# Kernel tuning notes

Measured on AMD Instinct MI355X. Metric: run time of the kernel, lower is better.

Reference implementation:

```python
import jax, jax.numpy as jnp
import numpy as np

R, TR = 47, 2  # response_size, treat_size


def _lstm_cell(x, h, c, Wih, Whh, bih, bhh):
    # PyTorch gate order: i, f, g, o
    gates = x @ Wih.T + h @ Whh.T + bih + bhh
    i, f, g, o = jnp.split(gates, 4, axis=-1)
    c_new = jax.nn.sigmoid(f) * c + jax.nn.sigmoid(i) * jnp.tanh(g)
    h_new = jax.nn.sigmoid(o) * jnp.tanh(c_new)
    return h_new, c_new


def setup_inputs() -> dict:
    key = jax.random.key(0)
    B, T = 256, 2048
    ks = jax.random.split(key, 20)

    def u(k, shape, H):
        s = 1.0 / np.sqrt(H).astype(np.float32)
        return jax.random.uniform(k, shape, jnp.float32, -s, s)

    return {
        "x_r": jax.random.normal(ks[0], (B, T, R), jnp.float32),
        "x_t": jax.random.normal(ks[1], (B, T, TR), jnp.float32),
        # r_rnn: 2-layer LSTM, input 49 -> hidden 47
        "r_Wih0": u(ks[2], (4 * R, R + TR), R), "r_Whh0": u(ks[3], (4 * R, R), R),
        "r_bih0": u(ks[4], (4 * R,), R), "r_bhh0": u(ks[5], (4 * R,), R),
        "r_Wih1": u(ks[6], (4 * R, R), R), "r_Whh1": u(ks[7], (4 * R, R), R),
        "r_bih1": u(ks[8], (4 * R,), R), "r_bhh1": u(ks[9], (4 * R,), R),
        # t_rnn: 2-layer LSTM, input 96 -> hidden 2
        "t_Wih0": u(ks[10], (4 * TR, 2 * R + TR), TR), "t_Whh0": u(ks[11], (4 * TR, TR), TR),
        "t_bih0": u(ks[12], (4 * TR,), TR), "t_bhh0": u(ks[13], (4 * TR,), TR),
        "t_Wih1": u(ks[14], (4 * TR, TR), TR), "t_Whh1": u(ks[15], (4 * TR, TR), TR),
        "t_bih1": u(ks[16], (4 * TR,), TR), "t_bhh1": u(ks[17], (4 * TR,), TR),
    }


def reference(x_r, x_t,
              r_Wih0, r_Whh0, r_bih0, r_bhh0, r_Wih1, r_Whh1, r_bih1, r_bhh1,
              t_Wih0, t_Whh0, t_bih0, t_bhh0, t_Wih1, t_Whh1, t_bih1, t_bhh1):
    B = x_r.shape[0]
    zR = jnp.zeros((B, R), x_r.dtype)
    zT = jnp.zeros((B, TR), x_r.dtype)

    def step(carry, xs):
        hr0, cr0, hr1, cr1, ht0, ct0, ht1, ct1 = carry
        r, t = xs  # [B,47], [B,2]
        r_in = jnp.concatenate([r, t], axis=-1)              # [B,49]
        hr0, cr0 = _lstm_cell(r_in, hr0, cr0, r_Wih0, r_Whh0, r_bih0, r_bhh0)
        hr1, cr1 = _lstm_cell(hr0, hr1, cr1, r_Wih1, r_Whh1, r_bih1, r_bhh1)
        t_in = jnp.concatenate([r_in, hr1], axis=-1)         # [B,96]
        ht0, ct0 = _lstm_cell(t_in, ht0, ct0, t_Wih0, t_Whh0, t_bih0, t_bhh0)
        ht1, ct1 = _lstm_cell(ht0, ht1, ct1, t_Wih1, t_Whh1, t_bih1, t_bhh1)
        return (hr0, cr0, hr1, cr1, ht0, ct0, ht1, ct1), (hr1, ht1)

    init = (zR, zR, zR, zR, zT, zT, zT, zT)
    xs = (x_r.transpose(1, 0, 2), x_t.transpose(1, 0, 2))    # time-major
    _, (r_seq, t_seq) = jax.lax.scan(step, init, xs)         # [T,B,47], [T,B,2]
    return (r_seq.transpose(1, 0, 2), t_seq.transpose(1, 0, 2))
```

## Files before the change

### kernel.cpp

```cpp
#include <hip/hip_runtime.h>

#define T_STEPS 2048
#define TOTAL   2080

typedef float f2 __attribute__((ext_vector_type(2)));
typedef _Float16 h2 __attribute__((ext_vector_type(2)));

__device__ __forceinline__ float fast_rcp(float x) { return __builtin_amdgcn_rcpf(x); }

__device__ __forceinline__ float sig_f(float x) { return fast_rcp(1.0f + __expf(-x)); }
__device__ __forceinline__ float tanh_f(float x) {
    float e = __expf(-2.0f * x);
    return fmaf(2.0f, fast_rcp(1.0f + e), -1.0f);
}
__device__ __forceinline__ float gate_act(float x, float zm, float sm, float sa) {
    float e = __expf(-x * zm);
    return fmaf(fast_rcp(1.0f + e), sm, sa);
}

#if __has_builtin(__builtin_amdgcn_fdot2)
#define FDOT2(a, b, c) __builtin_amdgcn_fdot2((a), (b), (c), false)
#else
__device__ __forceinline__ float FDOT2(h2 a, h2 b, float c) {
    return fmaf((float)a.x, (float)b.x, fmaf((float)a.y, (float)b.y, c));
}
#endif

#define LDS_BARRIER() asm volatile("s_waitcnt lgkmcnt(0)\n\ts_barrier" ::: "memory")

#define DPP_BCAST0 0x00
#define DPP_BCAST1 0x55
#define DPP_BCAST2 0xAA
#define DPP_BCAST3 0xFF
#define DPP_PAIR   0xF5
#define DPP_ROR4   0x124
#define DPP_ROR8   0x128
template<int CTRL>
__device__ __forceinline__ float dppf(float x) {
    int r = __builtin_amdgcn_update_dpp(0, __builtin_bit_cast(int, x), CTRL, 0xF, 0xF, true);
    return __builtin_bit_cast(float, r);
}

__device__ __forceinline__ void loadx4(float (&dst)[4], const float* __restrict__ x_r,
                                       const float* __restrict__ x_t,
                                       size_t xrb, size_t xtb, int l) {
#pragma unroll
    for (int u = 0; u < 4; ++u) {
        int v = l + 16 * u;
        dst[u] = (v < 47) ? x_r[xrb + v] : ((v < 49) ? x_t[xtb + (v - 47)] : 0.0f);
    }
}

__device__ __forceinline__ void unpack12(f2 (&in)[24], const float4* __restrict__ r4) {
#pragma unroll
    for (int u = 0; u < 12; ++u) {
        float4 v = r4[u];
        in[2 * u]     = f2{v.x, v.y};
        in[2 * u + 1] = f2{v.z, v.w};
    }
}

__device__ __forceinline__ void unpackh(h2 (&in)[24], const h2* __restrict__ row) {
    const float4* q = (const float4*)row;
#pragma unroll
    for (int k = 0; k < 6; ++k) {
        float4 v = q[k];
        in[4 * k + 0] = __builtin_bit_cast(h2, v.x);
        in[4 * k + 1] = __builtin_bit_cast(h2, v.y);
        in[4 * k + 2] = __builtin_bit_cast(h2, v.z);
        in[4 * k + 3] = __builtin_bit_cast(h2, v.w);
    }
}

__device__ __forceinline__ float4 dot4h(const h2 (&in)[24], const h2 (&w)[4][24], float4 init) {
    float a0 = init.x, a1 = init.y, a2 = init.z, a3 = init.w;
#pragma unroll
    for (int u = 0; u < 24; ++u) {
        a0 = FDOT2(w[0][u], in[u], a0);
        a1 = FDOT2(w[1][u], in[u], a1);
        a2 = FDOT2(w[2][u], in[u], a2);
        a3 = FDOT2(w[3][u], in[u], a3);
    }
    return float4{a0, a1, a2, a3};
}

__device__ __forceinline__ void loadw47h(h2 (&w)[24], const float* __restrict__ src) {
#pragma unroll
    for (int u = 0; u < 23; ++u)
        w[u] = h2{(_Float16)src[2 * u], (_Float16)src[2 * u + 1]};
    w[23] = h2{(_Float16)src[46], (_Float16)0.0f};
}

__global__ __launch_bounds__(256) void adrnn_fused(
    const float* __restrict__ x_r, const float* __restrict__ x_t,
    const float* __restrict__ rWih0, const float* __restrict__ rWhh0,
    const float* __restrict__ rbih0, const float* __restrict__ rbhh0,
    const float* __restrict__ rWih1, const float* __restrict__ rWhh1,
    const float* __restrict__ rbih1, const float* __restrict__ rbhh1,
    const float* __restrict__ tWih0, const float* __restrict__ tWhh0,
    const float* __restrict__ tbih0, const float* __restrict__ tbhh0,
    const float* __restrict__ tWih1, const float* __restrict__ tWhh1,
    const float* __restrict__ tbih1, const float* __restrict__ tbhh1,
    float* __restrict__ r_out, float* __restrict__ t_out)
{
    __shared__ __align__(16) float tring[64][112];
    __shared__ __align__(16) h2 h0f16[16][32];
    __shared__ __align__(16) h2 h1f16[16][32];
    __shared__ __align__(16) float pAring[16][192];
    __shared__ __align__(16) float pBring[16][192];

    const int tid = threadIdx.x;
    const int wid = tid >> 6;
    const int l   = tid & 63;
    const int j   = l;
    const int b = blockIdx.x;
    const size_t xr_base = (size_t)b * T_STEPS * 47;
    const size_t xt_base = (size_t)b * T_STEPS * 2;

    {
        for (int k = tid; k < 64 * 48; k += 256) tring[k / 48][64 + (k % 48)] = 0.0f;
        for (int k = tid; k < 16 * 32; k += 256) {
            h0f16[k >> 5][k & 31] = h2{(_Float16)0.0f, (_Float16)0.0f};
            h1f16[k >> 5][k & 31] = h2{(_Float16)0.0f, (_Float16)0.0f};
        }
    }

    if (wid == 0) {
        f2 w[4][24]; float w48[4]; float4 bias = {0, 0, 0, 0};
#pragma unroll
        for (int g = 0; g < 4; ++g) { w48[g] = 0.f;
#pragma unroll
            for (int u = 0; u < 24; ++u) w[g][u] = f2{0.f, 0.f}; }
        if (j < 47) {
            float bb[4];
#pragma unroll
            for (int g = 0; g < 4; ++g) {
                const int row = g * 47 + j;
#pragma unroll
                for (int u = 0; u < 24; ++u)
                    w[g][u] = f2{rWih0[row * 49 + 2 * u], rWih0[row * 49 + 2 * u + 1]};
                w48[g] = rWih0[row * 49 + 48];
                bb[g] = rbih0[row] + rbhh0[row];
            }
            bias = {bb[0], bb[1], bb[2], bb[3]};
        }
        float xa[4] = {0,0,0,0}, xb[4] = {0,0,0,0}, xc[4] = {0,0,0,0};
        if (l < 16) {
            for (int t = 0; t < 8; ++t) {
                float xv[4];
                loadx4(xv, x_r, x_t, xr_base + (size_t)t * 47, xt_base + (size_t)t * 2, l);
#pragma unroll
                for (int uu = 0; uu < 4; ++uu) {
                    int v = l + 16 * uu;
                    if (v < 49) tring[t][v] = xv[uu];
                }
            }
            loadx4(xa, x_r, x_t, xr_base + (size_t)8 * 47,  xt_base + (size_t)8 * 2,  l);
            loadx4(xb, x_r, x_t, xr_base + (size_t)9 * 47,  xt_base + (size_t)9 * 2,  l);
            loadx4(xc, x_r, x_t, xr_base + (size_t)10 * 47, xt_base + (size_t)10 * 2, l);
        }
        __syncthreads();
        for (int i = 0; i < TOTAL; ++i) {
            if (i < T_STEPS && j < 47) {
                f2 in[24];
                unpack12(in, (const float4*)&tring[i & 63][0]);
                float x48 = tring[i & 63][48];
                f2 a0 = f2{bias.x, 0.f}, b0v = {0, 0};
                f2 a1 = f2{bias.y, 0.f}, b1v = {0, 0};
                f2 a2 = f2{bias.z, 0.f}, b2v = {0, 0};
                f2 a3 = f2{bias.w, 0.f}, b3v = {0, 0};
#pragma unroll
                for (int u = 0; u < 12; ++u) {
                    a0  = __builtin_elementwise_fma(w[0][u],      in[u],      a0);
                    b0v = __builtin_elementwise_fma(w[0][12 + u], in[12 + u], b0v);
                    a1  = __builtin_elementwise_fma(w[1][u],      in[u],      a1);
                    b1v = __builtin_elementwise_fma(w[1][12 + u], in[12 + u], b1v);
                    a2  = __builtin_elementwise_fma(w[2][u],      in[u],      a2);
                    b2v = __builtin_elementwise_fma(w[2][12 + u], in[12 + u], b2v);
                    a3  = __builtin_elementwise_fma(w[3][u],      in[u],      a3);
                    b3v = __builtin_elementwise_fma(w[3][12 + u], in[12 + u], b3v);
                }
                f2 s0 = a0 + b0v, s1 = a1 + b1v, s2 = a2 + b2v, s3 = a3 + b3v;
                float4 out;
                out.x = fmaf(w48[0], x48, s0.x + s0.y);
                out.y = fmaf(w48[1], x48, s1.x + s1.y);
                out.z = fmaf(w48[2], x48, s2.x + s2.y);
                out.w = fmaf(w48[3], x48, s3.x + s3.y);
                *(float4*)&pAring[i & 15][j * 4] = out;
            }
            if (l < 16) {
                const int tw = i + 8;
                if (tw < T_STEPS) {
#pragma unroll
                    for (int uu = 0; uu < 4; ++uu) {
                        int v = l + 16 * uu;
                        if (v < 49) tring[tw & 63][v] = xa[uu];
                    }
                }
#pragma unroll
                for (int uu = 0; uu < 4; ++uu) { xa[uu] = xb[uu]; xb[uu] = xc[uu]; }
                int tl = i + 11;
                if (tl > T_STEPS - 1) tl = T_STEPS - 1;
                loadx4(xc, x_r, x_t, xr_base + (size_t)tl * 47, xt_base + (size_t)tl * 2, l);
            }
            if ((i & 7) == 7) LDS_BARRIER();
        }
    } else if (wid == 1) {
        h2 w[4][24];
#pragma unroll
        for (int g = 0; g < 4; ++g)
#pragma unroll
            for (int u = 0; u < 24; ++u) w[g][u] = h2{(_Float16)0.0f, (_Float16)0.0f};
        if (j < 47) {
#pragma unroll
            for (int g = 0; g < 4; ++g) loadw47h(w[g], &rWhh0[(g * 47 + j) * 47]);
        }
        float c0 = 0.f;
        __syncthreads();
        for (int i = 0; i < TOTAL; ++i) {
            const int s = i - 8;
            float hv = 0.0f;
            if (s >= 0 && s < T_STEPS && j < 47) {
                float4 pa = *(const float4*)&pAring[s & 15][j * 4];
                h2 in[24];
                unpackh(in, &h0f16[(s - 1) & 15][0]);
                float4 pre = dot4h(in, w, pa);
                float iv = sig_f(pre.x), fv = sig_f(pre.y);
                float gv = tanh_f(pre.z), ov = sig_f(pre.w);
                c0 = fmaf(fv, c0, iv * gv);
                hv = ov * tanh_f(c0);
            }
            float hn = dppf<DPP_PAIR>(hv);
            if (s >= 0 && s < T_STEPS && j < 47 && !(j & 1)) {
                h0f16[s & 15][j >> 1] = __builtin_bit_cast(h2, __builtin_amdgcn_cvt_pkrtz(hv, hn));
            }
            if ((i & 7) == 7) LDS_BARRIER();
        }
    } else if (wid == 2) {
        h2 w[4][24]; float4 bias = {0, 0, 0, 0};
#pragma unroll
        for (int g = 0; g < 4; ++g)
#pragma unroll
            for (int u = 0; u < 24; ++u) w[g][u] = h2{(_Float16)0.0f, (_Float16)0.0f};
        if (j < 47) {
            float bb[4];
#pragma unroll
            for (int g = 0; g < 4; ++g) {
                loadw47h(w[g], &rWih1[(g * 47 + j) * 47]);
                bb[g] = rbih1[g * 47 + j] + rbhh1[g * 47 + j];
            }
            bias = {bb[0], bb[1], bb[2], bb[3]};
        }
        const int tu  = (l >> 2) & 1;
        const int tg  = l & 3;
        const int thf = (l >> 3) & 1;
        const int R0 = tg * 2 + tu;
        f2 wt[24]; float wx48;
        if (thf == 0) {
            wx48 = 0.f;
#pragma unroll
            for (int k = 0; k < 24; ++k)
                wt[k] = f2{tWih0[R0 * 96 + 2 * k], tWih0[R0 * 96 + 2 * k + 1]};
        } else {
            wx48 = tWih0[R0 * 96 + 48];
#pragma unroll
            for (int k = 0; k < 23; ++k)
                wt[k] = f2{tWih0[R0 * 96 + 49 + 2 * k], tWih0[R0 * 96 + 49 + 2 * k + 1]};
            wt[23] = f2{tWih0[R0 * 96 + 95], 0.f};
        }
        const float bT0 = tbih0[R0] + tbhh0[R0];
        const float wh00 = tWhh0[R0 * 2 + 0], wh01 = tWhh0[R0 * 2 + 1];
        const float wi10 = tWih1[R0 * 2 + 0], wi11 = tWih1[R0 * 2 + 1];
        const float wh10 = tWhh1[R0 * 2 + 0], wh11 = tWhh1[R0 * 2 + 1];
        const float bT1 = tbih1[R0] + tbhh1[R0];
        const bool isg = (tg == 2);
        const float zm = isg ? 2.f : 1.f, sm = isg ? 2.f : 1.f, sa = isg ? -1.f : 0.f;
        float ht00 = 0.f, ht01 = 0.f, ct0u = 0.f;
        float ht10 = 0.f, ht11 = 0.f, ct1u = 0.f;

        __syncthreads();
        for (int i = 0; i < TOTAL; ++i) {
            const int s2 = i - 16;
            if (s2 >= 0 && s2 < T_STEPS && j < 47) {
                h2 in[24];
                unpackh(in, &h0f16[s2 & 15][0]);
                float4 pre = dot4h(in, w, bias);
                *(float4*)&pBring[s2 & 15][j * 4] = pre;
            }
            const int s = i - 32;
            if (s >= 0 && s < T_STEPS) {
                f2 in[24];
                unpack12(in, (const float4*)&tring[s & 63][thf ? 64 : 0]);
                float x48 = tring[s & 63][48];
                f2 av = {0, 0}, bv = {0, 0};
#pragma unroll
                for (int k = 0; k < 12; ++k) {
                    av = __builtin_elementwise_fma(wt[2 * k],     in[2 * k],     av);
                    bv = __builtin_elementwise_fma(wt[2 * k + 1], in[2 * k + 1], bv);
                }
                f2 sv = av + bv;
                float part = fmaf(wx48, x48, sv.x + sv.y);
                float pre0 = part + dppf<DPP_ROR8>(part);
                pre0 += bT0 + wh00 * ht00 + wh01 * ht01;
                float a0 = gate_act(pre0, zm, sm, sa);
                float i0 = dppf<DPP_BCAST0>(a0);
                float f0 = dppf<DPP_BCAST1>(a0);
                float g0 = dppf<DPP_BCAST2>(a0);
                float o0 = dppf<DPP_BCAST3>(a0);
                ct0u = fmaf(f0, ct0u, i0 * g0);
                float htu = o0 * tanh_f(ct0u);
                float hto = dppf<DPP_ROR4>(htu);
                ht00 = (tu == 0) ? htu : hto;
                ht01 = (tu == 0) ? hto : htu;
                float pre1 = bT1 + wi10 * ht00 + wi11 * ht01 + wh10 * ht10 + wh11 * ht11;
                float a1 = gate_act(pre1, zm, sm, sa);
                float ji = dppf<DPP_BCAST0>(a1);
                float jf = dppf<DPP_BCAST1>(a1);
                float jg = dppf<DPP_BCAST2>(a1);
                float jo = dppf<DPP_BCAST3>(a1);
                ct1u = fmaf(jf, ct1u, ji * jg);
                float h1u = jo * tanh_f(ct1u);
                float h1o = dppf<DPP_ROR4>(h1u);
                ht10 = (tu == 0) ? h1u : h1o;
                ht11 = (tu == 0) ? h1o : h1u;
                if (l == 0) {
                    float2 tv = {ht10, ht11};
                    *reinterpret_cast<float2*>(&t_out[((size_t)b * T_STEPS + s) * 2]) = tv;
                }
            }
            if ((i & 7) == 7) LDS_BARRIER();
        }
    } else {
        h2 w[4][24];
#pragma unroll
        for (int g = 0; g < 4; ++g)
#pragma unroll
            for (int u = 0; u < 24; ++u) w[g][u] = h2{(_Float16)0.0f, (_Float16)0.0f};
        if (j < 47) {
#pragma unroll
            for (int g = 0; g < 4; ++g) loadw47h(w[g], &rWhh1[(g * 47 + j) * 47]);
        }
        float c1 = 0.f;
        __syncthreads();
        for (int i = 0; i < TOTAL; ++i) {
            const int s = i - 24;
            float hv = 0.0f;
            if (s >= 0 && s < T_STEPS && j < 47) {
                float4 pb = *(const float4*)&pBring[s & 15][j * 4];
                h2 in[24];
                unpackh(in, &h1f16[(s - 1) & 15][0]);
                float4 pre = dot4h(in, w, pb);
                float iv = sig_f(pre.x), fv = sig_f(pre.y);
                float gv = tanh_f(pre.z), ov = sig_f(pre.w);
                c1 = fmaf(fv, c1, iv * gv);
                hv = ov * tanh_f(c1);
                tring[s & 63][64 + j] = hv;
                r_out[((size_t)b * T_STEPS + s) * 47 + j] = hv;
            }
            float hn = dppf<DPP_PAIR>(hv);
            if (s >= 0 && s < T_STEPS && j < 47 && !(j & 1)) {
                h1f16[s & 15][j >> 1] = __builtin_bit_cast(h2, __builtin_amdgcn_cvt_pkrtz(hv, hn));
            }
            if ((i & 7) == 7) LDS_BARRIER();
        }
    }
}

extern "C" void kernel_launch(void* const* d_in, const int* in_sizes, int n_in,
                              void* d_out, int out_size, void* d_ws, size_t ws_size,
                              hipStream_t stream) {
    const float* x_r   = (const float*)d_in[0];
    const float* x_t   = (const float*)d_in[1];
    const float* rWih0 = (const float*)d_in[2];
    const float* rWhh0 = (const float*)d_in[3];
    const float* rbih0 = (const float*)d_in[4];
    const float* rbhh0 = (const float*)d_in[5];
    const float* rWih1 = (const float*)d_in[6];
    const float* rWhh1 = (const float*)d_in[7];
    const float* rbih1 = (const float*)d_in[8];
    const float* rbhh1 = (const float*)d_in[9];
    const float* tWih0 = (const float*)d_in[10];
    const float* tWhh0 = (const float*)d_in[11];
    const float* tbih0 = (const float*)d_in[12];
    const float* tbhh0 = (const float*)d_in[13];
    const float* tWih1 = (const float*)d_in[14];
    const float* tWhh1 = (const float*)d_in[15];
    const float* tbih1 = (const float*)d_in[16];
    const float* tbhh1 = (const float*)d_in[17];

    float* r_out = (float*)d_out;
    float* t_out = r_out + (size_t)256 * T_STEPS * 47;

    hipLaunchKernelGGL(adrnn_fused, dim3(256), dim3(256), 0, stream,
                       x_r, x_t, rWih0, rWhh0, rbih0, rbhh0, rWih1, rWhh1, rbih1, rbhh1,
                       tWih0, tWhh0, tbih0, tbhh0, tWih1, tWhh1, tbih1, tbhh1,
                       r_out, t_out);
}
```

Measured before the change: 1.452 ms.

## Collapse four-wave LSTM pipeline into three waves with fused per-layer dot products

Restructures the block from four wavefronts (input projection, layer-0 recurrence, layer-1 input projection, layer-1 recurrence plus t_rnn) into three. Each r_rnn layer wave now computes both its input and hidden products itself in fp16 fdot2, and the t_rnn wave also handles the x prefetch ring, now stored as packed fp16. This removes the pAring/pBring staging buffers and shortens the pipeline depth (TOTAL 2080 to 2064). The cost is a longer serial dependency chain per layer step and extra fp16 rounding of inputs and of the t_rnn weights.

```diff
diff --git a/kernel.cpp b/kernel.cpp
--- a/kernel.cpp
+++ b/kernel.cpp
@@ -1,13 +1,12 @@
 #include <hip/hip_runtime.h>
 
 #define T_STEPS 2048
-#define TOTAL   2080
+#define TOTAL   2064
 
 typedef float f2 __attribute__((ext_vector_type(2)));
 typedef _Float16 h2 __attribute__((ext_vector_type(2)));
 
 __device__ __forceinline__ float fast_rcp(float x) { return __builtin_amdgcn_rcpf(x); }
-
 __device__ __forceinline__ float sig_f(float x) { return fast_rcp(1.0f + __expf(-x)); }
 __device__ __forceinline__ float tanh_f(float x) {
     float e = __expf(-2.0f * x);
@@ -41,23 +40,8 @@
     return __builtin_bit_cast(float, r);
 }
 
-__device__ __forceinline__ void loadx4(float (&dst)[4], const float* __restrict__ x_r,
-                                       const float* __restrict__ x_t,
-                                       size_t xrb, size_t xtb, int l) {
-#pragma unroll
-    for (int u = 0; u < 4; ++u) {
-        int v = l + 16 * u;
-        dst[u] = (v < 47) ? x_r[xrb + v] : ((v < 49) ? x_t[xtb + (v - 47)] : 0.0f);
-    }
-}
-
-__device__ __forceinline__ void unpack12(f2 (&in)[24], const float4* __restrict__ r4) {
-#pragma unroll
-    for (int u = 0; u < 12; ++u) {
-        float4 v = r4[u];
-        in[2 * u]     = f2{v.x, v.y};
-        in[2 * u + 1] = f2{v.z, v.w};
-    }
+__device__ __forceinline__ h2 pk16(float a, float b) {
+    return __builtin_bit_cast(h2, __builtin_amdgcn_cvt_pkrtz(a, b));
 }
 
 __device__ __forceinline__ void unpackh(h2 (&in)[24], const h2* __restrict__ row) {
@@ -71,17 +55,16 @@
         in[4 * k + 3] = __builtin_bit_cast(h2, v.w);
     }
 }
-
-__device__ __forceinline__ float4 dot4h(const h2 (&in)[24], const h2 (&w)[4][24], float4 init) {
-    float a0 = init.x, a1 = init.y, a2 = init.z, a3 = init.w;
-#pragma unroll
-    for (int u = 0; u < 24; ++u) {
-        a0 = FDOT2(w[0][u], in[u], a0);
-        a1 = FDOT2(w[1][u], in[u], a1);
-        a2 = FDOT2(w[2][u], in[u], a2);
-        a3 = FDOT2(w[3][u], in[u], a3);
-    }
-    return float4{a0, a1, a2, a3};
+__device__ __forceinline__ void unpackx(h2 (&in)[28], const h2* __restrict__ row) {
+    const float4* q = (const float4*)row;
+#pragma unroll
+    for (int k = 0; k < 7; ++k) {
+        float4 v = q[k];
+        in[4 * k + 0] = __builtin_bit_cast(h2, v.x);
+        in[4 * k + 1] = __builtin_bit_cast(h2, v.y);
+        in[4 * k + 2] = __builtin_bit_cast(h2, v.z);
+        in[4 * k + 3] = __builtin_bit_cast(h2, v.w);
+    }
 }
 
 __device__ __forceinline__ void loadw47h(h2 (&w)[24], const float* __restrict__ src) {
@@ -90,8 +73,24 @@
         w[u] = h2{(_Float16)src[2 * u], (_Float16)src[2 * u + 1]};
     w[23] = h2{(_Float16)src[46], (_Float16)0.0f};
 }
-
-__global__ __launch_bounds__(256) void adrnn_fused(
+__device__ __forceinline__ void loadw49h(h2 (&w)[25], const float* __restrict__ src) {
+#pragma unroll
+    for (int u = 0; u < 24; ++u)
+        w[u] = h2{(_Float16)src[2 * u], (_Float16)src[2 * u + 1]};
+    w[24] = h2{(_Float16)src[48], (_Float16)0.0f};
+}
+
+__device__ __forceinline__ void loadx4c(float (&dst)[4], const float* __restrict__ x_r,
+                                        const float* __restrict__ x_t,
+                                        size_t xrb, size_t xtb, int k) {
+#pragma unroll
+    for (int m = 0; m < 4; ++m) {
+        int v = 4 * k + m;
+        dst[m] = (v < 47) ? x_r[xrb + v] : ((v < 49) ? x_t[xtb + (v - 47)] : 0.0f);
+    }
+}
+
+__global__ __launch_bounds__(192) void adrnn_fused(
     const float* __restrict__ x_r, const float* __restrict__ x_t,
     const float* __restrict__ rWih0, const float* __restrict__ rWhh0,
     const float* __restrict__ rbih0, const float* __restrict__ rbhh0,
@@ -103,11 +102,9 @@
     const float* __restrict__ tbih1, const float* __restrict__ tbhh1,
     float* __restrict__ r_out, float* __restrict__ t_out)
 {
-    __shared__ __align__(16) float tring[64][112];
-    __shared__ __align__(16) h2 h0f16[16][32];
-    __shared__ __align__(16) h2 h1f16[16][32];
-    __shared__ __align__(16) float pAring[16][192];
-    __shared__ __align__(16) float pBring[16][192];
+    __shared__ __align__(16) h2 xring[32][28];
+    __shared__ __align__(16) h2 h0f16[16][24];
+    __shared__ __align__(16) h2 h1f16[16][24];
 
     const int tid = threadIdx.x;
     const int wid = tid >> 6;
@@ -117,156 +114,133 @@
     const size_t xr_base = (size_t)b * T_STEPS * 47;
     const size_t xt_base = (size_t)b * T_STEPS * 2;
 
-    {
-        for (int k = tid; k < 64 * 48; k += 256) tring[k / 48][64 + (k % 48)] = 0.0f;
-        for (int k = tid; k < 16 * 32; k += 256) {
-            h0f16[k >> 5][k & 31] = h2{(_Float16)0.0f, (_Float16)0.0f};
-            h1f16[k >> 5][k & 31] = h2{(_Float16)0.0f, (_Float16)0.0f};
-        }
+    for (int k = tid; k < 16 * 24; k += 192) {
+        h0f16[k / 24][k % 24] = h2{(_Float16)0.0f, (_Float16)0.0f};
+        h1f16[k / 24][k % 24] = h2{(_Float16)0.0f, (_Float16)0.0f};
     }
 
     if (wid == 0) {
-        f2 w[4][24]; float w48[4]; float4 bias = {0, 0, 0, 0};
-#pragma unroll
-        for (int g = 0; g < 4; ++g) { w48[g] = 0.f;
-#pragma unroll
-            for (int u = 0; u < 24; ++u) w[g][u] = f2{0.f, 0.f}; }
+        h2 wx[4][25]; h2 wh[4][24]; float bias[4] = {0, 0, 0, 0};
+#pragma unroll
+        for (int g = 0; g < 4; ++g) {
+#pragma unroll
+            for (int u = 0; u < 25; ++u) wx[g][u] = h2{(_Float16)0.0f, (_Float16)0.0f};
+#pragma unroll
+            for (int u = 0; u < 24; ++u) wh[g][u] = h2{(_Float16)0.0f, (_Float16)0.0f};
+        }
         if (j < 47) {
-            float bb[4];
 #pragma unroll
             for (int g = 0; g < 4; ++g) {
                 const int row = g * 47 + j;
-#pragma unroll
-                for (int u = 0; u < 24; ++u)
-                    w[g][u] = f2{rWih0[row * 49 + 2 * u], rWih0[row * 49 + 2 * u + 1]};
-                w48[g] = rWih0[row * 49 + 48];
-                bb[g] = rbih0[row] + rbhh0[row];
-            }
-            bias = {bb[0], bb[1], bb[2], bb[3]};
-        }
-        float xa[4] = {0,0,0,0}, xb[4] = {0,0,0,0}, xc[4] = {0,0,0,0};
-        if (l < 16) {
-            for (int t = 0; t < 8; ++t) {
-                float xv[4];
-                loadx4(xv, x_r, x_t, xr_base + (size_t)t * 47, xt_base + (size_t)t * 2, l);
-#pragma unroll
-                for (int uu = 0; uu < 4; ++uu) {
-                    int v = l + 16 * uu;
-                    if (v < 49) tring[t][v] = xv[uu];
-                }
-            }
-            loadx4(xa, x_r, x_t, xr_base + (size_t)8 * 47,  xt_base + (size_t)8 * 2,  l);
-            loadx4(xb, x_r, x_t, xr_base + (size_t)9 * 47,  xt_base + (size_t)9 * 2,  l);
-            loadx4(xc, x_r, x_t, xr_base + (size_t)10 * 47, xt_base + (size_t)10 * 2, l);
-        }
+                loadw49h(wx[g], &rWih0[row * 49]);
+                loadw47h(wh[g], &rWhh0[row * 47]);
+                bias[g] = rbih0[row] + rbhh0[row];
+            }
+        }
+        float c0 = 0.f;
         __syncthreads();
         for (int i = 0; i < TOTAL; ++i) {
+            float hv = 0.0f;
             if (i < T_STEPS && j < 47) {
-                f2 in[24];
-                unpack12(in, (const float4*)&tring[i & 63][0]);
-                float x48 = tring[i & 63][48];
-                f2 a0 = f2{bias.x, 0.f}, b0v = {0, 0};
-                f2 a1 = f2{bias.y, 0.f}, b1v = {0, 0};
-                f2 a2 = f2{bias.z, 0.f}, b2v = {0, 0};
-                f2 a3 = f2{bias.w, 0.f}, b3v = {0, 0};
-#pragma unroll
-                for (int u = 0; u < 12; ++u) {
-                    a0  = __builtin_elementwise_fma(w[0][u],      in[u],      a0);
-                    b0v = __builtin_elementwise_fma(w[0][12 + u], in[12 + u], b0v);
-                    a1  = __builtin_elementwise_fma(w[1][u],      in[u],      a1);
-                    b1v = __builtin_elementwise_fma(w[1][12 + u], in[12 + u], b1v);
-                    a2  = __builtin_elementwise_fma(w[2][u],      in[u],      a2);
-                    b2v = __builtin_elementwise_fma(w[2][12 + u], in[12 + u], b2v);
-                    a3  = __builtin_elementwise_fma(w[3][u],      in[u],      a3);
-                    b3v = __builtin_elementwise_fma(w[3][12 + u], in[12 + u], b3v);
-                }
-                f2 s0 = a0 + b0v, s1 = a1 + b1v, s2 = a2 + b2v, s3 = a3 + b3v;
-                float4 out;
-                out.x = fmaf(w48[0], x48, s0.x + s0.y);
-                out.y = fmaf(w48[1], x48, s1.x + s1.y);
-                out.z = fmaf(w48[2], x48, s2.x + s2.y);
-                out.w = fmaf(w48[3], x48, s3.x + s3.y);
-                *(float4*)&pAring[i & 15][j * 4] = out;
-            }
-            if (l < 16) {
-                const int tw = i + 8;
-                if (tw < T_STEPS) {
-#pragma unroll
-                    for (int uu = 0; uu < 4; ++uu) {
-                        int v = l + 16 * uu;
-                        if (v < 49) tring[tw & 63][v] = xa[uu];
-                    }
-                }
-#pragma unroll
-                for (int uu = 0; uu < 4; ++uu) { xa[uu] = xb[uu]; xb[uu] = xc[uu]; }
-                int tl = i + 11;
-                if (tl > T_STEPS - 1) tl = T_STEPS - 1;
-                loadx4(xc, x_r, x_t, xr_base + (size_t)tl * 47, xt_base + (size_t)tl * 2, l);
-            }
+                h2 xin[28];
+                unpackx(xin, &xring[i & 31][0]);
+                h2 hin[24];
+                unpackh(hin, &h0f16[(i - 1) & 15][0]);
+                float a0 = bias[0], a1 = bias[1], a2 = bias[2], a3 = bias[3];
+#pragma unroll
+                for (int u = 0; u < 25; ++u) {
+                    a0 = FDOT2(wx[0][u], xin[u], a0);
+                    a1 = FDOT2(wx[1][u], xin[u], a1);
+                    a2 = FDOT2(wx[2][u], xin[u], a2);
+                    a3 = FDOT2(wx[3][u], xin[u], a3);
+                }
+#pragma unroll
+                for (int u = 0; u < 24; ++u) {
+                    a0 = FDOT2(wh[0][u], hin[u], a0);
+                    a1 = FDOT2(wh[1][u], hin[u], a1);
+                    a2 = FDOT2(wh[2][u], hin[u], a2);
+                    a3 = FDOT2(wh[3][u], hin[u], a3);
+                }
+                float iv = sig_f(a0), fv = sig_f(a1);
+                float gv = tanh_f(a2), ov = sig_f(a3);
+                c0 = fmaf(fv, c0, iv * gv);
+                hv = ov * tanh_f(c0);
+            }
+            float hn = dppf<DPP_PAIR>(hv);
+            if (i < T_STEPS && j < 47 && !(j & 1)) h0f16[i & 15][j >> 1] = pk16(hv, hn);
             if ((i & 7) == 7) LDS_BARRIER();
         }
     } else if (wid == 1) {
-        h2 w[4][24];
-#pragma unroll
-        for (int g = 0; g < 4; ++g)
-#pragma unroll
-            for (int u = 0; u < 24; ++u) w[g][u] = h2{(_Float16)0.0f, (_Float16)0.0f};
+        h2 wx[4][24]; h2 wh[4][24]; float bias[4] = {0, 0, 0, 0};
+#pragma unroll
+        for (int g = 0; g < 4; ++g) {
+#pragma unroll
+            for (int u = 0; u < 24; ++u) {
+                wx[g][u] = h2{(_Float16)0.0f, (_Float16)0.0f};
+                wh[g][u] = h2{(_Float16)0.0f, (_Float16)0.0f};
+            }
+        }
         if (j < 47) {
 #pragma unroll
-            for (int g = 0; g < 4; ++g) loadw47h(w[g], &rWhh0[(g * 47 + j) * 47]);
-        }
-        float c0 = 0.f;
+            for (int g = 0; g < 4; ++g) {
+                const int row = g * 47 + j;
+                loadw47h(wx[g], &rWih1[row * 47]);
+                loadw47h(wh[g], &rWhh1[row * 47]);
+                bias[g] = rbih1[row] + rbhh1[row];
+            }
+        }
+        float c1 = 0.f;
         __syncthreads();
         for (int i = 0; i < TOTAL; ++i) {
             const int s = i - 8;
             float hv = 0.0f;
             if (s >= 0 && s < T_STEPS && j < 47) {
-                float4 pa = *(const float4*)&pAring[s & 15][j * 4];
-                h2 in[24];
-                unpackh(in, &h0f16[(s - 1) & 15][0]);
-                float4 pre = dot4h(in, w, pa);
-                float iv = sig_f(pre.x), fv = sig_f(pre.y);
-                float gv = tanh_f(pre.z), ov = sig_f(pre.w);
-                c0 = fmaf(fv, c0, iv * gv);
-                hv = ov * tanh_f(c0);
+                h2 xin[24];
+                unpackh(xin, &h0f16[s & 15][0]);
+                h2 hin[24];
+                unpackh(hin, &h1f16[(s - 1) & 15][0]);
+                float a0 = bias[0], a1 = bias[1], a2 = bias[2], a3 = bias[3];
+#pragma unroll
+                for (int u = 0; u < 24; ++u) {
+                    a0 = FDOT2(wx[0][u], xin[u], a0);
+                    a1 = FDOT2(wx[1][u], xin[u], a1);
+                    a2 = FDOT2(wx[2][u], xin[u], a2);
+                    a3 = FDOT2(wx[3][u], xin[u], a3);
+                }
+#pragma unroll
+                for (int u = 0; u < 24; ++u) {
+                    a0 = FDOT2(wh[0][u], hin[u], a0);
+                    a1 = FDOT2(wh[1][u], hin[u], a1);
+                    a2 = FDOT2(wh[2][u], hin[u], a2);
+                    a3 = FDOT2(wh[3][u], hin[u], a3);
+                }
+                float iv = sig_f(a0), fv = sig_f(a1);
+                float gv = tanh_f(a2), ov = sig_f(a3);
+                c1 = fmaf(fv, c1, iv * gv);
+                hv = ov * tanh_f(c1);
+                r_out[((size_t)b * T_STEPS + s) * 47 + j] = hv;
             }
             float hn = dppf<DPP_PAIR>(hv);
-            if (s >= 0 && s < T_STEPS && j < 47 && !(j & 1)) {
-                h0f16[s & 15][j >> 1] = __builtin_bit_cast(h2, __builtin_amdgcn_cvt_pkrtz(hv, hn));
-            }
+            if (s >= 0 && s < T_STEPS && j < 47 && !(j & 1)) h1f16[s & 15][j >> 1] = pk16(hv, hn);
             if ((i & 7) == 7) LDS_BARRIER();
         }
-    } else if (wid == 2) {
-        h2 w[4][24]; float4 bias = {0, 0, 0, 0};
-#pragma unroll
-        for (int g = 0; g < 4; ++g)
-#pragma unroll
-            for (int u = 0; u < 24; ++u) w[g][u] = h2{(_Float16)0.0f, (_Float16)0.0f};
-        if (j < 47) {
-            float bb[4];
-#pragma unroll
-            for (int g = 0; g < 4; ++g) {
-                loadw47h(w[g], &rWih1[(g * 47 + j) * 47]);
-                bb[g] = rbih1[g * 47 + j] + rbhh1[g * 47 + j];
-            }
-            bias = {bb[0], bb[1], bb[2], bb[3]};
-        }
+    } else {
         const int tu  = (l >> 2) & 1;
         const int tg  = l & 3;
         const int thf = (l >> 3) & 1;
         const int R0 = tg * 2 + tu;
-        f2 wt[24]; float wx48;
+        h2 wt[24]; float wx48;
         if (thf == 0) {
             wx48 = 0.f;
 #pragma unroll
-            for (int k = 0; k < 24; ++k)
-                wt[k] = f2{tWih0[R0 * 96 + 2 * k], tWih0[R0 * 96 + 2 * k + 1]};
+            for (int u = 0; u < 24; ++u)
+                wt[u] = h2{(_Float16)tWih0[R0 * 96 + 2 * u], (_Float16)tWih0[R0 * 96 + 2 * u + 1]};
         } else {
             wx48 = tWih0[R0 * 96 + 48];
 #pragma unroll
-            for (int k = 0; k < 23; ++k)
-                wt[k] = f2{tWih0[R0 * 96 + 49 + 2 * k], tWih0[R0 * 96 + 49 + 2 * k + 1]};
-            wt[23] = f2{tWih0[R0 * 96 + 95], 0.f};
+            for (int u = 0; u < 23; ++u)
+                wt[u] = h2{(_Float16)tWih0[R0 * 96 + 49 + 2 * u], (_Float16)tWih0[R0 * 96 + 49 + 2 * u + 1]};
+            wt[23] = h2{(_Float16)tWih0[R0 * 96 + 95], (_Float16)0.0f};
         }
         const float bT0 = tbih0[R0] + tbhh0[R0];
         const float wh00 = tWhh0[R0 * 2 + 0], wh01 = tWhh0[R0 * 2 + 1];
@@ -278,28 +252,43 @@
         float ht00 = 0.f, ht01 = 0.f, ct0u = 0.f;
         float ht10 = 0.f, ht11 = 0.f, ct1u = 0.f;
 
+        float xa[4] = {0,0,0,0}, xb[4] = {0,0,0,0}, xc[4] = {0,0,0,0};
+        if (l < 13) {
+            for (int t = 0; t < 8; ++t) {
+                float xv[4];
+                loadx4c(xv, x_r, x_t, xr_base + (size_t)t * 47, xt_base + (size_t)t * 2, l);
+                xring[t][2 * l]     = pk16(xv[0], xv[1]);
+                xring[t][2 * l + 1] = pk16(xv[2], xv[3]);
+            }
+            loadx4c(xa, x_r, x_t, xr_base + (size_t)8 * 47,  xt_base + (size_t)8 * 2,  l);
+            loadx4c(xb, x_r, x_t, xr_base + (size_t)9 * 47,  xt_base + (size_t)9 * 2,  l);
+            loadx4c(xc, x_r, x_t, xr_base + (size_t)10 * 47, xt_base + (size_t)10 * 2, l);
+        }
         __syncthreads();
+
         for (int i = 0; i < TOTAL; ++i) {
-            const int s2 = i - 16;
-            if (s2 >= 0 && s2 < T_STEPS && j < 47) {
-                h2 in[24];
-                unpackh(in, &h0f16[s2 & 15][0]);
-                float4 pre = dot4h(in, w, bias);
-                *(float4*)&pBring[s2 & 15][j * 4] = pre;
-            }
-            const int s = i - 32;
+            if (l < 13) {
+                const int tw = i + 8;
+                if (tw < T_STEPS) {
+                    xring[tw & 31][2 * l]     = pk16(xa[0], xa[1]);
+                    xring[tw & 31][2 * l + 1] = pk16(xa[2], xa[3]);
+                }
+#pragma unroll
+                for (int m = 0; m < 4; ++m) { xa[m] = xb[m]; xb[m] = xc[m]; }
+                int tl = i + 11;
+                if (tl > T_STEPS - 1) tl = T_STEPS - 1;
+                loadx4c(xc, x_r, x_t, xr_base + (size_t)tl * 47, xt_base + (size_t)tl * 2, l);
+            }
+            const int s = i - 16;
             if (s >= 0 && s < T_STEPS) {
-                f2 in[24];
-                unpack12(in, (const float4*)&tring[s & 63][thf ? 64 : 0]);
-                float x48 = tring[s & 63][48];
-                f2 av = {0, 0}, bv = {0, 0};
-#pragma unroll
-                for (int k = 0; k < 12; ++k) {
-                    av = __builtin_elementwise_fma(wt[2 * k],     in[2 * k],     av);
-                    bv = __builtin_elementwise_fma(wt[2 * k + 1], in[2 * k + 1], bv);
-                }
-                f2 sv = av + bv;
-                float part = fmaf(wx48, x48, sv.x + sv.y);
+                const h2* src = (thf == 0) ? &xring[s & 31][0] : &h1f16[s & 15][0];
+                h2 tin[24];
+                unpackh(tin, src);
+                float x48v = (float)xring[s & 31][24].x;
+                float acc = 0.f;
+#pragma unroll
+                for (int u = 0; u < 24; ++u) acc = FDOT2(wt[u], tin[u], acc);
+                float part = (thf == 1) ? fmaf(wx48, x48v, acc) : acc;
                 float pre0 = part + dppf<DPP_ROR8>(part);
                 pre0 += bT0 + wh00 * ht00 + wh01 * ht01;
                 float a0 = gate_act(pre0, zm, sm, sa);
@@ -330,39 +319,6 @@
             }
             if ((i & 7) == 7) LDS_BARRIER();
         }
-    } else {
-        h2 w[4][24];
-#pragma unroll
-        for (int g = 0; g < 4; ++g)
-#pragma unroll
-            for (int u = 0; u < 24; ++u) w[g][u] = h2{(_Float16)0.0f, (_Float16)0.0f};
-        if (j < 47) {
-#pragma unroll
-            for (int g = 0; g < 4; ++g) loadw47h(w[g], &rWhh1[(g * 47 + j) * 47]);
-        }
-        float c1 = 0.f;
-        __syncthreads();
-        for (int i = 0; i < TOTAL; ++i) {
-            const int s = i - 24;
-            float hv = 0.0f;
-            if (s >= 0 && s < T_STEPS && j < 47) {
-                float4 pb = *(const float4*)&pBring[s & 15][j * 4];
-                h2 in[24];
-                unpackh(in, &h1f16[(s - 1) & 15][0]);
-                float4 pre = dot4h(in, w, pb);
-                float iv = sig_f(pre.x), fv = sig_f(pre.y);
-                float gv = tanh_f(pre.z), ov = sig_f(pre.w);
-                c1 = fmaf(fv, c1, iv * gv);
-                hv = ov * tanh_f(c1);
-                tring[s & 63][64 + j] = hv;
-                r_out[((size_t)b * T_STEPS + s) * 47 + j] = hv;
-            }
-            float hn = dppf<DPP_PAIR>(hv);
-            if (s >= 0 && s < T_STEPS && j < 47 && !(j & 1)) {
-                h1f16[s & 15][j >> 1] = __builtin_bit_cast(h2, __builtin_amdgcn_cvt_pkrtz(hv, hn));
-            }
-            if ((i & 7) == 7) LDS_BARRIER();
-        }
     }
 }
 
@@ -391,7 +347,7 @@
     float* r_out = (float*)d_out;
     float* t_out = r_out + (size_t)256 * T_STEPS * 47;
 
-    hipLaunchKernelGGL(adrnn_fused, dim3(256), dim3(256), 0, stream,
+    hipLaunchKernelGGL(adrnn_fused, dim3(256), dim3(192), 0, stream,
                        x_r, x_t, rWih0, rWhh0, rbih0, rbhh0, rWih1, rWhh1, rbih1, rbhh1,
                        tWih0, tWhh0, tbih0, tbhh0, tWih1, tWhh1, tbih1, tbhh1,
                        r_out, t_out);
```

After: 1.277 ms. 1.14x faster.
